# Kernel optimization log

Measured on AMD Instinct MI355X. Metric: run time of the kernel, lower is better.

The kernel has to match this reference:

```python
import jax, jax.numpy as jnp
import numpy as np

N = 512          # atoms
MAX_DIST = 16    # shortest-path truncation
N_HEADS = 32
N_SPATIAL = 64
BOND_TYPES = 32  # bond_types_number global in original repo


def setup_inputs() -> dict:
    key = jax.random.key(0)
    k1, k2, k3, k4, k5 = jax.random.split(key, 5)
    spatial_pos = jax.random.randint(k1, (N, N), 0, N_SPATIAL, dtype=jnp.int32)
    edge_input = jax.random.randint(k2, (N, N, MAX_DIST), 0, BOND_TYPES, dtype=jnp.int32)
    # embedding tables; padding_idx=0 -> zero row 0
    spd_table = jax.random.normal(k3, (N_SPATIAL, N_HEADS), dtype=jnp.float32).at[0].set(0.0)
    edge_table = jax.random.normal(k4, (BOND_TYPES, N_HEADS), dtype=jnp.float32).at[0].set(0.0)
    edge_dis_weight = jax.random.normal(k5, (N_SPATIAL * N_HEADS * N_HEADS, 1), dtype=jnp.float32)
    return {
        "spatial_pos": spatial_pos,
        "edge_input": edge_input,
        "max_dist": MAX_DIST,
        "spd_table": spd_table,
        "edge_table": edge_table,
        "edge_dis_weight": edge_dis_weight,
    }


def reference(spatial_pos, edge_input, max_dist, spd_table, edge_table, edge_dis_weight):
    n_heads = spd_table.shape[1]
    # phi_spd: embedding gather [n,n,H] -> [H,n,n]
    phi_spd = jnp.transpose(spd_table[spatial_pos], (2, 0, 1))
    # edge embedding gather: [n,n,D,H]
    edge_emb = edge_table[edge_input]
    # per-distance HxH weight matrices: [D,H,H]
    W = edge_dis_weight.reshape(-1, n_heads, n_heads)[:max_dist]
    # fused per-hop bmm + sum over hops: sum_d edge_emb[i,j,d,:] @ W[d]  -> [n,n,H]
    edge_sum = jnp.einsum('ijdh,dhk->ijk', edge_emb, W)
    # divide by clamped shortest-path distance (0 -> 1)
    denom = jnp.where(spatial_pos == 0, 1, spatial_pos).astype(edge_sum.dtype)[..., None]
    phi_edge = jnp.transpose(edge_sum / denom, (2, 0, 1))
    return (phi_spd, phi_edge)
```

## Files before the change

kernel.cpp:

```cpp
#include <hip/hip_runtime.h>
#include <stdint.h>

#define NH 32

__device__ __forceinline__ float bf_to_f(uint16_t u)
{
    return __uint_as_float(((uint32_t)u) << 16);
}

__device__ __forceinline__ void cp16(const void* g, void* l)
{
    __builtin_amdgcn_global_load_lds(
        (const __attribute__((address_space(1))) void*)g,
        (__attribute__((address_space(3))) void*)l, 16, 0, 0);
}

__device__ __forceinline__ int block_detect_fp32(const uint16_t* p16, int tid,
                                                 int* s_flag)
{
    if (tid == 0) *s_flag = 0;
    __syncthreads();
    const ushort4* p = (const ushort4*)p16;
    ushort4 a = p[tid * 2];
    ushort4 b = p[tid * 2 + 1];
    int big = 0;
    big |= (((a.x >> 7) & 0xFF) >= 0x89); big |= (((a.y >> 7) & 0xFF) >= 0x89);
    big |= (((a.z >> 7) & 0xFF) >= 0x89); big |= (((a.w >> 7) & 0xFF) >= 0x89);
    big |= (((b.x >> 7) & 0xFF) >= 0x89); big |= (((b.y >> 7) & 0xFF) >= 0x89);
    big |= (((b.z >> 7) & 0xFF) >= 0x89); big |= (((b.w >> 7) & 0xFF) >= 0x89);
    if (big) atomicOr(s_flag, 1);
    __syncthreads();
    return *s_flag;
}

__global__ __launch_bounds__(256) void prep(
    const void* __restrict__ edge_table,
    const void* __restrict__ W,
    const void* __restrict__ spd,
    float* __restrict__ T,
    float* __restrict__ spdT,
    int totalT, int spd_n)
{
    __shared__ int s_flag;
    const int tid = threadIdx.x;
    const int is_fp32 = block_detect_fp32((const uint16_t*)spd, tid, &s_flag);
    int g = blockIdx.x * 256 + tid;
    if (g < totalT) {
        int d = g >> 10, e = (g >> 5) & 31, k = g & 31;
        float acc = 0.f;
        if (is_fp32) {
            const float* et = (const float*)edge_table + e * NH;
            const float* w  = (const float*)W + d * NH * NH + k;
#pragma unroll
            for (int h = 0; h < NH; ++h) acc += et[h] * w[h * NH];
        } else {
            const uint16_t* et = (const uint16_t*)edge_table + e * NH;
            const uint16_t* w  = (const uint16_t*)W + d * NH * NH + k;
#pragma unroll
            for (int h = 0; h < NH; ++h) acc += bf_to_f(et[h]) * bf_to_f(w[h * NH]);
        }
        int k4 = (k >> 2) ^ (e & 7);
        T[(d << 10) | (e << 5) | (k4 << 2) | (k & 3)] = acc;
    } else {
        int i = g - totalT;
        if (i < spd_n) {
            float v = is_fp32 ? ((const float*)spd)[i]
                              : bf_to_f(((const uint16_t*)spd)[i]);
            int s = i >> 5, h = i & 31;
            spdT[h * (spd_n >> 5) + s] = v;
        }
    }
}

__global__ __launch_bounds__(256, 4) void bond2d(
    const int* __restrict__ spatial,
    const int* __restrict__ edge,
    const float4* __restrict__ SgT,
    const float4* __restrict__ Tg,
    float* __restrict__ out,
    int npairs, int D, int ns)
{
    __shared__ float4 Tl[2048];
    __shared__ float4 Sl4[512];
    float* Sl = (float*)Sl4;

    const int t  = threadIdx.x;
    const int p0 = blockIdx.x * 256 + t;
    const bool valid = (p0 < npairs);
    const int p  = valid ? p0 : 0;

    const int s_val = spatial[p];

    const int nsf4 = (NH * ns) >> 2;
    for (int i = t; i < nsf4; i += 256)
        cp16(SgT + i, Sl4 + i);

    float acc[32];
#pragma unroll
    for (int k = 0; k < 32; ++k) acc[k] = 0.f;

    const int* erow = edge + (size_t)p * D;

    for (int c0 = 0; c0 < D; c0 += 8) {
        const int dlen = (D - c0 < 8) ? (D - c0) : 8;
        if (c0) __syncthreads();
        if (dlen == 8) {
#pragma unroll
            for (int i = 0; i < 8; ++i)
                cp16(Tg + (c0 + i) * 256 + t, Tl + i * 256 + t);
            int4 q0 = *(const int4*)(erow + c0);
            int4 q1 = *(const int4*)(erow + c0 + 4);
            __syncthreads();
            int ev[8] = {q0.x, q0.y, q0.z, q0.w, q1.x, q1.y, q1.z, q1.w};
#pragma unroll
            for (int d = 0; d < 8; ++d) {
                int e = ev[d];
                int boff = (d << 12) + (e << 7) + ((e & 7) << 4);
#pragma unroll
                for (int m = 0; m < 8; ++m) {
                    float4 v = *(const float4*)((const char*)Tl + (boff ^ (m << 4)));
                    acc[4*m+0] += v.x; acc[4*m+1] += v.y;
                    acc[4*m+2] += v.z; acc[4*m+3] += v.w;
                }
            }
        } else {
            for (int i = t; i < dlen * 256; i += 256)
                cp16(Tg + c0 * 256 + i, Tl + i);
            __syncthreads();
            for (int d = 0; d < dlen; ++d) {
                int e = erow[c0 + d];
                int boff = (d << 12) + (e << 7) + ((e & 7) << 4);
#pragma unroll
                for (int m = 0; m < 8; ++m) {
                    float4 v = *(const float4*)((const char*)Tl + (boff ^ (m << 4)));
                    acc[4*m+0] += v.x; acc[4*m+1] += v.y;
                    acc[4*m+2] += v.z; acc[4*m+3] += v.w;
                }
            }
        }
    }

    if (!valid) return;

    const float rs = 1.0f / (s_val ? (float)s_val : 1.0f);
    float* o0 = out + p0;
    float* o1 = out + (size_t)NH * npairs + p0;
    const float* sA = Sl + s_val;
#pragma unroll
    for (int k = 0; k < 32; ++k) {
        o1[k * npairs] = acc[k] * rs;
        o0[k * npairs] = sA[k * ns];
    }
}

extern "C" void kernel_launch(void* const* d_in, const int* in_sizes, int n_in,
                              void* d_out, int out_size, void* d_ws, size_t ws_size,
                              hipStream_t stream) {
    const int* spatial = (const int*)d_in[0];
    const int* edge    = (const int*)d_in[1];
    const void* spd    = d_in[3];
    const void* etab   = d_in[4];
    const void* W      = d_in[5];

    long long npairs = in_sizes[0];
    long long etot   = in_sizes[1];
    int D = (int)(etot / (npairs > 0 ? npairs : 1));
    if (D < 1) D = 1;
    if (D > 64) D = 64;
    int spd_n  = in_sizes[3];
    int ns     = spd_n >> 5;
    int totalT = D * 1024;

    float* T    = (float*)d_ws;
    float* spdT = T + totalT;

    prep<<<(totalT + spd_n + 255) / 256, 256, 0, stream>>>(
        etab, W, spd, T, spdT, totalT, spd_n);

    int nblk = (int)((npairs + 255) / 256);
    bond2d<<<nblk, 256, 0, stream>>>(spatial, edge, (const float4*)spdT,
                                     (const float4*)T, (float*)d_out,
                                     (int)npairs, D, ns);
}
```

Measured before the change: 104.4 us.

## Split output heads across two blocks per pair tile to halve accumulators

Each pair tile now runs as two blocks, each handling 16 of the 32 heads. The fused table is re-laid out per head-half with a new XOR swizzle, and hops are staged 16 at a time. Outputs are written interleaved with the final accumulation, and the spd table slice is staged in LDS only when it is small. The aim is fewer registers, higher occupancy and more blocks in flight, at the cost of reading edge indices and spatial values twice.

```diff
diff --git a/kernel.cpp b/kernel.cpp
--- a/kernel.cpp
+++ b/kernel.cpp
@@ -39,7 +39,7 @@
     const void* __restrict__ spd,
     float* __restrict__ T,
     float* __restrict__ spdT,
-    int totalT, int spd_n)
+    int totalT, int spd_n, int D)
 {
     __shared__ int s_flag;
     const int tid = threadIdx.x;
@@ -59,8 +59,11 @@
 #pragma unroll
             for (int h = 0; h < NH; ++h) acc += bf_to_f(et[h]) * bf_to_f(w[h * NH]);
         }
-        int k4 = (k >> 2) ^ (e & 7);
-        T[(d << 10) | (e << 5) | (k4 << 2) | (k & 3)] = acc;
+        int khalf = k >> 4;
+        int grp   = (k >> 2) & 3;
+        int idx = ((khalf * D + d) * 32 + e) * 16
+                + ((grp ^ ((e >> 1) & 3)) << 2) + (k & 3);
+        T[idx] = acc;
     } else {
         int i = g - totalT;
         if (i < spd_n) {
@@ -80,76 +83,99 @@
     float* __restrict__ out,
     int npairs, int D, int ns)
 {
-    __shared__ float4 Tl[2048];
-    __shared__ float4 Sl4[512];
-    float* Sl = (float*)Sl4;
-
-    const int t  = threadIdx.x;
-    const int p0 = blockIdx.x * 256 + t;
+    __shared__ float4 Tl4[2048];
+    __shared__ float4 Sl4[256];
+    const float* Sl = (const float*)Sl4;
+
+    const int t     = threadIdx.x;
+    const int pblk  = blockIdx.x >> 1;
+    const int khalf = blockIdx.x & 1;
+    const int p0    = pblk * 256 + t;
     const bool valid = (p0 < npairs);
-    const int p  = valid ? p0 : 0;
+    const int p     = valid ? p0 : 0;
 
     const int s_val = spatial[p];
-
-    const int nsf4 = (NH * ns) >> 2;
-    for (int i = t; i < nsf4; i += 256)
-        cp16(SgT + i, Sl4 + i);
-
-    float acc[32];
-#pragma unroll
-    for (int k = 0; k < 32; ++k) acc[k] = 0.f;
-
-    const int* erow = edge + (size_t)p * D;
-
-    for (int c0 = 0; c0 < D; c0 += 8) {
-        const int dlen = (D - c0 < 8) ? (D - c0) : 8;
-        if (c0) __syncthreads();
-        if (dlen == 8) {
-#pragma unroll
-            for (int i = 0; i < 8; ++i)
-                cp16(Tg + (c0 + i) * 256 + t, Tl + i * 256 + t);
-            int4 q0 = *(const int4*)(erow + c0);
-            int4 q1 = *(const int4*)(erow + c0 + 4);
-            __syncthreads();
-            int ev[8] = {q0.x, q0.y, q0.z, q0.w, q1.x, q1.y, q1.z, q1.w};
-#pragma unroll
-            for (int d = 0; d < 8; ++d) {
-                int e = ev[d];
-                int boff = (d << 12) + (e << 7) + ((e & 7) << 4);
-#pragma unroll
-                for (int m = 0; m < 8; ++m) {
-                    float4 v = *(const float4*)((const char*)Tl + (boff ^ (m << 4)));
-                    acc[4*m+0] += v.x; acc[4*m+1] += v.y;
-                    acc[4*m+2] += v.z; acc[4*m+3] += v.w;
-                }
-            }
-        } else {
-            for (int i = t; i < dlen * 256; i += 256)
-                cp16(Tg + c0 * 256 + i, Tl + i);
-            __syncthreads();
-            for (int d = 0; d < dlen; ++d) {
-                int e = erow[c0 + d];
-                int boff = (d << 12) + (e << 7) + ((e & 7) << 4);
-#pragma unroll
-                for (int m = 0; m < 8; ++m) {
-                    float4 v = *(const float4*)((const char*)Tl + (boff ^ (m << 4)));
-                    acc[4*m+0] += v.x; acc[4*m+1] += v.y;
-                    acc[4*m+2] += v.z; acc[4*m+3] += v.w;
-                }
-            }
-        }
-    }
-
-    if (!valid) return;
+    const bool small_ns = (ns <= 64);
+
+    if (small_ns && t < 4 * ns)
+        cp16(SgT + khalf * 4 * ns + t, Sl4 + t);
+
+    float acc[16];
+#pragma unroll
+    for (int k = 0; k < 16; ++k) acc[k] = 0.f;
+
+    const int* erow  = edge + (size_t)p * D;
+    const int  Tbase = khalf * D * 128;
 
     const float rs = 1.0f / (s_val ? (float)s_val : 1.0f);
     float* o0 = out + p0;
     float* o1 = out + (size_t)NH * npairs + p0;
-    const float* sA = Sl + s_val;
-#pragma unroll
-    for (int k = 0; k < 32; ++k) {
-        o1[k * npairs] = acc[k] * rs;
-        o0[k * npairs] = sA[k * ns];
+
+    for (int c0 = 0; c0 < D; c0 += 16) {
+        const int dlen = (D - c0 < 16) ? (D - c0) : 16;
+        if (c0) __syncthreads();
+        int ev[16];
+        if (dlen == 16) {
+#pragma unroll
+            for (int i = 0; i < 8; ++i)
+                cp16(Tg + Tbase + c0 * 128 + i * 256 + t, Tl4 + i * 256 + t);
+            int4 q0 = *(const int4*)(erow + c0);
+            int4 q1 = *(const int4*)(erow + c0 + 4);
+            int4 q2 = *(const int4*)(erow + c0 + 8);
+            int4 q3 = *(const int4*)(erow + c0 + 12);
+            ev[0]=q0.x;  ev[1]=q0.y;  ev[2]=q0.z;  ev[3]=q0.w;
+            ev[4]=q1.x;  ev[5]=q1.y;  ev[6]=q1.z;  ev[7]=q1.w;
+            ev[8]=q2.x;  ev[9]=q2.y;  ev[10]=q2.z; ev[11]=q2.w;
+            ev[12]=q3.x; ev[13]=q3.y; ev[14]=q3.z; ev[15]=q3.w;
+        } else {
+            for (int i = t; i < dlen * 128; i += 256)
+                cp16(Tg + Tbase + c0 * 128 + i, Tl4 + i);
+            for (int d = 0; d < dlen; ++d) ev[d] = erow[c0 + d];
+            for (int d = dlen; d < 16; ++d) ev[d] = 0;
+        }
+        __syncthreads();
+
+        const char* Tb = (const char*)Tl4;
+        const bool last = (c0 + 16 >= D);
+#pragma unroll
+        for (int o = 0; o < 2; ++o) {
+            if (dlen == 16) {
+#pragma unroll
+                for (int d = 0; d < 16; ++d) {
+                    int e  = ev[d];
+                    int rb = (d << 11) + (e << 6);
+                    int sw = ((e >> 1) & 3) << 4;
+                    float4 v0 = *(const float4*)(Tb + rb + (((2*o  ) << 4) ^ sw));
+                    float4 v1 = *(const float4*)(Tb + rb + (((2*o+1) << 4) ^ sw));
+                    acc[8*o+0] += v0.x; acc[8*o+1] += v0.y;
+                    acc[8*o+2] += v0.z; acc[8*o+3] += v0.w;
+                    acc[8*o+4] += v1.x; acc[8*o+5] += v1.y;
+                    acc[8*o+6] += v1.z; acc[8*o+7] += v1.w;
+                }
+            } else {
+                for (int d = 0; d < dlen; ++d) {
+                    int e  = ev[d];
+                    int rb = (d << 11) + (e << 6);
+                    int sw = ((e >> 1) & 3) << 4;
+                    float4 v0 = *(const float4*)(Tb + rb + (((2*o  ) << 4) ^ sw));
+                    float4 v1 = *(const float4*)(Tb + rb + (((2*o+1) << 4) ^ sw));
+                    acc[8*o+0] += v0.x; acc[8*o+1] += v0.y;
+                    acc[8*o+2] += v0.z; acc[8*o+3] += v0.w;
+                    acc[8*o+4] += v1.x; acc[8*o+5] += v1.y;
+                    acc[8*o+6] += v1.z; acc[8*o+7] += v1.w;
+                }
+            }
+            if (last && valid) {
+                const int kb = khalf * 16 + 8 * o;
+#pragma unroll
+                for (int j = 0; j < 8; ++j) {
+                    o1[(size_t)(kb + j) * npairs] = acc[8*o+j] * rs;
+                    o0[(size_t)(kb + j) * npairs] =
+                        small_ns ? Sl[(8*o+j) * ns + s_val]
+                                 : ((const float*)SgT)[(size_t)(kb + j) * ns + s_val];
+                }
+            }
+        }
     }
 }
 
@@ -175,9 +201,9 @@
     float* spdT = T + totalT;
 
     prep<<<(totalT + spd_n + 255) / 256, 256, 0, stream>>>(
-        etab, W, spd, T, spdT, totalT, spd_n);
-
-    int nblk = (int)((npairs + 255) / 256);
+        etab, W, spd, T, spdT, totalT, spd_n, D);
+
+    int nblk = 2 * (int)((npairs + 255) / 256);
     bond2d<<<nblk, 256, 0, stream>>>(spatial, edge, (const float4*)spdT,
                                      (const float4*)T, (float*)d_out,
                                      (int)npairs, D, ns);
```

Result: slower. 169.7 us (+62.5%).

## Make bond2d persistent with full-table LDS load and prefetch of next tile's indices

Applied to the files above, without the earlier changes.

Changes bond2d into a persistent grid of at most 512 blocks. Each block loads the whole 16-hop transformed table (64KB) into LDS once, then loops over tiles of 256 pairs while prefetching the next tile's spatial and edge indices. This removes the per-8-hop chunked reload and the barriers inside the loop, and amortises the LDS fill across many tiles. In exchange, LDS use per block doubles and occupancy drops to 2 blocks per CU. D is now clamped to 16, so larger hop counts would be silently truncated.

```diff
diff --git a/kernel.cpp b/kernel.cpp
--- a/kernel.cpp
+++ b/kernel.cpp
@@ -72,48 +72,69 @@
     }
 }
 
-__global__ __launch_bounds__(256, 4) void bond2d(
+__global__ __launch_bounds__(256, 2) void bond2d(
     const int* __restrict__ spatial,
     const int* __restrict__ edge,
     const float4* __restrict__ SgT,
     const float4* __restrict__ Tg,
     float* __restrict__ out,
-    int npairs, int D, int ns)
-{
-    __shared__ float4 Tl[2048];
+    int npairs, int D, int ns, int ntiles, int gridsz)
+{
+    __shared__ float4 Tl[4096];
     __shared__ float4 Sl4[512];
-    float* Sl = (float*)Sl4;
-
-    const int t  = threadIdx.x;
-    const int p0 = blockIdx.x * 256 + t;
-    const bool valid = (p0 < npairs);
-    const int p  = valid ? p0 : 0;
-
-    const int s_val = spatial[p];
-
-    const int nsf4 = (NH * ns) >> 2;
-    for (int i = t; i < nsf4; i += 256)
-        cp16(SgT + i, Sl4 + i);
-
-    float acc[32];
-#pragma unroll
-    for (int k = 0; k < 32; ++k) acc[k] = 0.f;
-
-    const int* erow = edge + (size_t)p * D;
-
-    for (int c0 = 0; c0 < D; c0 += 8) {
-        const int dlen = (D - c0 < 8) ? (D - c0) : 8;
-        if (c0) __syncthreads();
-        if (dlen == 8) {
-#pragma unroll
-            for (int i = 0; i < 8; ++i)
-                cp16(Tg + (c0 + i) * 256 + t, Tl + i * 256 + t);
-            int4 q0 = *(const int4*)(erow + c0);
-            int4 q1 = *(const int4*)(erow + c0 + 4);
-            __syncthreads();
-            int ev[8] = {q0.x, q0.y, q0.z, q0.w, q1.x, q1.y, q1.z, q1.w};
-#pragma unroll
-            for (int d = 0; d < 8; ++d) {
+    const float* Sl = (const float*)Sl4;
+
+    const int t = threadIdx.x;
+    const bool small_ns = (ns <= 64);
+
+    for (int i = t; i < D * 256; i += 256)
+        cp16(Tg + i, Tl + i);
+    if (small_ns) {
+        const int nsf4 = (NH * ns) >> 2;
+        for (int i = t; i < nsf4; i += 256)
+            cp16(SgT + i, Sl4 + i);
+    }
+
+    int tile = blockIdx.x;
+    int  pc  = tile * 256 + t;
+    bool vc  = (pc < npairs);
+    int  pcc = vc ? pc : 0;
+    int  sc  = spatial[pcc];
+    int4 c0, c1, c2, c3;
+    if (D == 16) {
+        const int4* er = (const int4*)(edge + (size_t)pcc * 16);
+        c0 = er[0]; c1 = er[1]; c2 = er[2]; c3 = er[3];
+    }
+
+    __syncthreads();
+
+    if (D == 16) {
+        for (;;) {
+            const int  tn  = tile + gridsz;
+            const bool hn  = (tn < ntiles);
+            int  pn = tn * 256 + t;
+            bool vn = hn && (pn < npairs);
+            int  pnn = vn ? pn : 0;
+            int  sn = 0;
+            int4 n0, n1, n2, n3;
+            if (hn) {
+                sn = spatial[pnn];
+                const int4* er = (const int4*)(edge + (size_t)pnn * 16);
+                n0 = er[0]; n1 = er[1]; n2 = er[2]; n3 = er[3];
+            }
+
+            int ev[16];
+            ev[0]=c0.x;  ev[1]=c0.y;  ev[2]=c0.z;  ev[3]=c0.w;
+            ev[4]=c1.x;  ev[5]=c1.y;  ev[6]=c1.z;  ev[7]=c1.w;
+            ev[8]=c2.x;  ev[9]=c2.y;  ev[10]=c2.z; ev[11]=c2.w;
+            ev[12]=c3.x; ev[13]=c3.y; ev[14]=c3.z; ev[15]=c3.w;
+
+            float acc[32];
+#pragma unroll
+            for (int k = 0; k < 32; ++k) acc[k] = 0.f;
+
+#pragma unroll
+            for (int d = 0; d < 16; ++d) {
                 int e = ev[d];
                 int boff = (d << 12) + (e << 7) + ((e & 7) << 4);
 #pragma unroll
@@ -123,33 +144,62 @@
                     acc[4*m+2] += v.z; acc[4*m+3] += v.w;
                 }
             }
-        } else {
-            for (int i = t; i < dlen * 256; i += 256)
-                cp16(Tg + c0 * 256 + i, Tl + i);
-            __syncthreads();
-            for (int d = 0; d < dlen; ++d) {
-                int e = erow[c0 + d];
+
+            if (vc) {
+                const float rs = 1.0f / (sc ? (float)sc : 1.0f);
+                float* o0 = out + pc;
+                float* o1 = out + (size_t)NH * npairs + pc;
+                const float* sA = Sl + sc;
+#pragma unroll
+                for (int k = 0; k < 32; ++k) {
+                    o1[(size_t)k * npairs] = acc[k] * rs;
+                    o0[(size_t)k * npairs] =
+                        small_ns ? sA[k * ns]
+                                 : ((const float*)SgT)[(size_t)k * ns + sc];
+                }
+            }
+
+            if (!hn) break;
+            tile = tn; pc = pn; vc = vn; pcc = pnn; sc = sn;
+            c0 = n0; c1 = n1; c2 = n2; c3 = n3;
+        }
+    } else {
+        for (; tile < ntiles; tile += gridsz) {
+            int  p  = tile * 256 + t;
+            bool v  = (p < npairs);
+            int  pp = v ? p : 0;
+            int  s  = spatial[pp];
+            const int* erow = edge + (size_t)pp * D;
+
+            float acc[32];
+#pragma unroll
+            for (int k = 0; k < 32; ++k) acc[k] = 0.f;
+
+            for (int d = 0; d < D; ++d) {
+                int e = erow[d];
                 int boff = (d << 12) + (e << 7) + ((e & 7) << 4);
 #pragma unroll
                 for (int m = 0; m < 8; ++m) {
-                    float4 v = *(const float4*)((const char*)Tl + (boff ^ (m << 4)));
-                    acc[4*m+0] += v.x; acc[4*m+1] += v.y;
-                    acc[4*m+2] += v.z; acc[4*m+3] += v.w;
-                }
-            }
-        }
-    }
-
-    if (!valid) return;
-
-    const float rs = 1.0f / (s_val ? (float)s_val : 1.0f);
-    float* o0 = out + p0;
-    float* o1 = out + (size_t)NH * npairs + p0;
-    const float* sA = Sl + s_val;
-#pragma unroll
-    for (int k = 0; k < 32; ++k) {
-        o1[k * npairs] = acc[k] * rs;
-        o0[k * npairs] = sA[k * ns];
+                    float4 vv = *(const float4*)((const char*)Tl + (boff ^ (m << 4)));
+                    acc[4*m+0] += vv.x; acc[4*m+1] += vv.y;
+                    acc[4*m+2] += vv.z; acc[4*m+3] += vv.w;
+                }
+            }
+
+            if (v) {
+                const float rs = 1.0f / (s ? (float)s : 1.0f);
+                float* o0 = out + p;
+                float* o1 = out + (size_t)NH * npairs + p;
+                const float* sA = Sl + s;
+#pragma unroll
+                for (int k = 0; k < 32; ++k) {
+                    o1[(size_t)k * npairs] = acc[k] * rs;
+                    o0[(size_t)k * npairs] =
+                        small_ns ? sA[k * ns]
+                                 : ((const float*)SgT)[(size_t)k * ns + s];
+                }
+            }
+        }
     }
 }
 
@@ -166,7 +216,7 @@
     long long etot   = in_sizes[1];
     int D = (int)(etot / (npairs > 0 ? npairs : 1));
     if (D < 1) D = 1;
-    if (D > 64) D = 64;
+    if (D > 16) D = 16;
     int spd_n  = in_sizes[3];
     int ns     = spd_n >> 5;
     int totalT = D * 1024;
@@ -177,8 +227,9 @@
     prep<<<(totalT + spd_n + 255) / 256, 256, 0, stream>>>(
         etab, W, spd, T, spdT, totalT, spd_n);
 
-    int nblk = (int)((npairs + 255) / 256);
-    bond2d<<<nblk, 256, 0, stream>>>(spatial, edge, (const float4*)spdT,
-                                     (const float4*)T, (float*)d_out,
-                                     (int)npairs, D, ns);
-}
+    int ntiles = (int)((npairs + 255) / 256);
+    int gridsz = ntiles < 512 ? ntiles : 512;
+    bond2d<<<gridsz, 256, 0, stream>>>(spatial, edge, (const float4*)spdT,
+                                       (const float4*)T, (float*)d_out,
+                                       (int)npairs, D, ns, ntiles, gridsz);
+}
```

Result: no change. 103.8 us (-0.6%).
